# Kernel tuning notes

Measured on AMD Instinct MI355X. Metric: run time of the kernel, lower is better.

The kernel has to match this reference:

```python
import jax, jax.numpy as jnp
import numpy as np

N_NODES = 20000
N_EDGES = 100000
WALK_LEN = 4
FEAT_DIM = 256
HID = 64
NUM_HEAD = 8
H_RNN = NUM_HEAD * HID  # 512
OUT_DIM = 16


def setup_inputs() -> dict:
    key = jax.random.key(0)
    ks = jax.random.split(key, 12)
    s = 0.05  # small init scale for numerical stability
    return {
        "x": jax.random.normal(ks[0], (N_NODES, FEAT_DIM), jnp.float32),
        "W_mlp": jax.random.normal(ks[1], (HID, FEAT_DIM), jnp.float32) * s,
        "b_mlp": jnp.zeros((HID,), jnp.float32),
        "W_ih": jax.random.normal(ks[2], (3 * H_RNN, HID), jnp.float32) * s,
        "W_hh": jax.random.normal(ks[3], (3 * H_RNN, H_RNN), jnp.float32) * s,
        "b_ih": jnp.zeros((3 * H_RNN,), jnp.float32),
        "b_hh": jnp.zeros((3 * H_RNN,), jnp.float32),
        "attn": jax.random.normal(ks[4], (1, NUM_HEAD, HID), jnp.float32) * s,
        "W_emb": jax.random.normal(ks[5], (HID, H_RNN), jnp.float32) * s,
        "b_emb": jnp.zeros((HID,), jnp.float32),
        "W_last": jax.random.normal(ks[6], (OUT_DIM, HID), jnp.float32) * s,
        "b_last": jnp.zeros((OUT_DIM,), jnp.float32),
        "edge_metapath_indices": jax.random.randint(ks[7], (N_EDGES, WALK_LEN), 0, N_NODES),
        "num_nodes": N_NODES,
    }


def reference(x, W_mlp, b_mlp, W_ih, W_hh, b_ih, b_hh, attn, W_emb, b_emb,
              W_last, b_last, edge_metapath_indices, num_nodes):
    # self channel: embedding = mlp(data.x)
    emb = x @ W_mlp.T + b_mlp                       # [N, hid]

    # rnn channel: gather per-metapath node embeddings
    edata = emb[edge_metapath_indices]              # [E, L, hid]
    E = edata.shape[0]
    h_rnn = W_hh.shape[1]

    # torch nn.GRU cell (gate order r, z, n), scan over path length
    def gru_step(h, x_t):
        xg = x_t @ W_ih.T + b_ih                    # [E, 3H]
        hg = h @ W_hh.T + b_hh                      # [E, 3H]
        xr, xz, xn = jnp.split(xg, 3, axis=-1)
        hr, hz, hn = jnp.split(hg, 3, axis=-1)
        r = jax.nn.sigmoid(xr + hr)
        z = jax.nn.sigmoid(xz + hz)
        n = jnp.tanh(xn + r * hn)
        return (1.0 - z) * n + z * h, None

    h0 = jnp.zeros((E, h_rnn), edata.dtype)
    hT, _ = jax.lax.scan(gru_step, h0, jnp.swapaxes(edata, 0, 1))  # [E, 8*hid]

    num_head, hid = attn.shape[1], attn.shape[2]
    eft = hT.reshape(E, num_head, hid)              # per-edge features

    # attention logits + leaky_relu(0.01)
    a = jnp.sum(eft * attn, axis=-1)                # [E, num_head]
    a = jnp.where(a > 0, a, 0.01 * a)

    # edge softmax grouped by destination node (indices[:, -1])
    dst = edge_metapath_indices[:, -1]
    m = jax.ops.segment_max(a, dst, num_segments=num_nodes)        # [N, H]
    ea = jnp.exp(a - m[dst])
    ssum = jax.ops.segment_sum(ea, dst, num_segments=num_nodes)    # [N, H]
    alpha = ea / ssum[dst]                          # [E, H]

    # message passing: scatter-sum of attention-weighted edge features
    ft = jax.ops.segment_sum(eft * alpha[:, :, None], dst,
                             num_segments=num_nodes)               # [N, H, hid]
    ret = ft.reshape(num_nodes, num_head * hid)
    rnn_emb = ret @ W_emb.T + b_emb                 # [N, hid]

    out = rnn_emb @ W_last.T + b_last               # [N, out_dim]
    return out
```

## Files before the change

kernel.cpp:

```cpp
#include <hip/hip_runtime.h>
#include <hip/hip_bf16.h>
#include <cstdint>

#define N_NODES 20000
#define N_EDGES 100000
#define WALK 4
#define FDIM 256
#define HID 64
#define NHEAD 8
#define HR 512
#define OUTD 16

typedef __attribute__((ext_vector_type(8))) short bf16x8;
typedef __attribute__((ext_vector_type(8))) unsigned short u16x8;
typedef __attribute__((ext_vector_type(4))) float f32x4;

__device__ __forceinline__ float b2f(unsigned short u){
  union{float f; unsigned u;} x; x.u = ((unsigned)u)<<16; return x.f;
}
__device__ __forceinline__ unsigned short f2b(float f){
  union{float f; unsigned u;} x; x.f = f;
  unsigned r = x.u + 0x7FFFu + ((x.u>>16)&1u);
  return (unsigned short)(r>>16);
}
__device__ __forceinline__ float sigmoidf_(float v){ return 1.0f/(1.0f+__expf(-v)); }
__device__ __forceinline__ float tanh_c(float v){
  v = fminf(fmaxf(v, -15.f), 15.f);
  const float t2 = __expf(2.0f*v);
  return (t2 - 1.0f) / (t2 + 1.0f);
}

__device__ __forceinline__ void gload16(const void* g, void* l){
  __builtin_amdgcn_global_load_lds(
      (const __attribute__((address_space(1))) void*)(g),
      (__attribute__((address_space(3))) void*)(l),
      16, 0, 0);
}

__device__ __forceinline__ f32x4 mfma16(bf16x8 a, bf16x8 b, f32x4 c){
  return __builtin_amdgcn_mfma_f32_16x16x32_bf16(a, b, c, 0, 0, 0);
}

__launch_bounds__(256)
__global__ void emb_kernel(const float* __restrict__ x,
                           const float* __restrict__ Wm,
                           const float* __restrict__ bm,
                           unsigned short* __restrict__ emb_bf)
{
  __shared__ float xs[4][FDIM];
  const int tid = threadIdx.x;
  const int node0 = blockIdx.x * 4;
  {
    const int row = tid >> 6;
    const int k4  = (tid & 63) * 4;
    *reinterpret_cast<float4*>(&xs[row][k4]) =
      *reinterpret_cast<const float4*>(&x[(size_t)(node0+row)*FDIM + k4]);
  }
  __syncthreads();
  const int nn = tid >> 6, c = tid & 63;
  float acc = bm[c];
  const float* wr = &Wm[c*FDIM];
  #pragma unroll 8
  for (int k=0;k<FDIM;k+=4){
    const float4 w = *reinterpret_cast<const float4*>(&wr[k]);
    acc += xs[nn][k]*w.x + xs[nn][k+1]*w.y + xs[nn][k+2]*w.z + xs[nn][k+3]*w.w;
  }
  emb_bf[(size_t)(node0+nn)*HID + c] = f2b(acc);
}

__launch_bounds__(256)
__global__ void prep_kernel(const float* __restrict__ Whh,
                            const float* __restrict__ Wih,
                            const float* __restrict__ Wemb,
                            unsigned short* __restrict__ WhhP,
                            unsigned short* __restrict__ WihP,
                            unsigned short* __restrict__ WembP)
{
  const int t = blockIdx.x*256 + threadIdx.x;
  if (t < 8*192*512){
    const int k = t & 511;
    const int r = (t >> 9) % 192;
    const int db = t / 98304;
    const int f = r >> 4, fr = r & 15;
    const int g = f % 3, dgrp = f / 3;
    const int G = g*HR + db*64 + dgrp*16 + fr;
    const int kg = k >> 6, kw = k & 63;
    const int c = kw >> 3, o = kw & 7;
    const int ksrc = (kg<<6) + (((c ^ (r&7)) << 3) | o);
    WhhP[t] = f2b(Whh[(size_t)G*HR + ksrc]);
  }
  if (t < 8*192*64){
    const int k = t & 63;
    const int r = (t >> 6) % 192;
    const int db = t / 12288;
    const int f = r >> 4, fr = r & 15;
    const int g = f % 3, dgrp = f / 3;
    const int G = g*HR + db*64 + dgrp*16 + fr;
    const int c = k >> 3, o = k & 7;
    const int ksrc = (((c ^ (r&7)) << 3) | o);
    WihP[t] = f2b(Wih[(size_t)G*HID + ksrc]);
  }
  if (t < 64*512){
    const int k = t & 511;
    const int o = t >> 9;
    const int kg = k >> 6, kw = k & 63;
    const int c = kw >> 3, off = kw & 7;
    const int ksrc = (kg<<6) + (((c ^ (o&7)) << 3) | off);
    WembP[t] = f2b(Wemb[(size_t)o*HR + ksrc]);
  }
}

__launch_bounds__(512)
__global__ void xg_kernel(const unsigned short* __restrict__ emb_bf,
                          const unsigned short* __restrict__ WihP,
                          const float* __restrict__ b_ih,
                          const float* __restrict__ b_hh,
                          unsigned short* __restrict__ xnP,
                          unsigned short* __restrict__ h1n)
{
  __shared__ __align__(16) char smem[32768 + 24576];
  char* Ab = smem;
  char* Bb = smem + 32768;
  const int tid = threadIdx.x, lane = tid & 63, w = tid >> 6;
  const int wr = w >> 1, wn = w & 1;
  const int n0 = blockIdx.x * 256;
  const int db = blockIdx.y;

  #pragma unroll
  for (int j=0;j<4;++j){
    const int flat = j*512 + tid;
    const int row = flat >> 3, c = flat & 7;
    int n = n0 + row; if (n > N_NODES-1) n = N_NODES-1;
    gload16(emb_bf + ((size_t)n*HID + ((c ^ (row&7))<<3)), Ab + ((j*512 + w*64)<<4));
  }
  #pragma unroll
  for (int j=0;j<3;++j){
    const int flat = j*512 + tid;
    const int row = flat >> 3, c = flat & 7;
    gload16(WihP + ((size_t)(db*192 + row)*HID + c*8), Bb + ((j*512 + w*64)<<4));
  }
  asm volatile("s_waitcnt vmcnt(0)" ::: "memory");
  __builtin_amdgcn_s_barrier();

  f32x4 acc[4][6];
  #pragma unroll
  for (int m=0;m<4;++m)
    #pragma unroll
    for (int f=0;f<6;++f) acc[m][f] = (f32x4)(0.f);

  auto readFrag = [&](const char* base, int row, int kk)->bf16x8{
    const int chunk = (kk<<2) + (lane>>4);
    return *reinterpret_cast<const bf16x8*>(base + (row<<7) + ((chunk ^ (row&7))<<4));
  };
  #pragma unroll
  for (int kk=0; kk<2; ++kk){
    bf16x8 a_[4];
    #pragma unroll
    for (int mf=0; mf<4; ++mf) a_[mf] = readFrag(Ab, wr*64 + mf*16 + (lane&15), kk);
    #pragma unroll
    for (int nf=0; nf<6; ++nf){
      const bf16x8 b_ = readFrag(Bb, wn*96 + nf*16 + (lane&15), kk);
      #pragma unroll
      for (int mf=0; mf<4; ++mf) acc[mf][nf] = mfma16(a_[mf], b_, acc[mf][nf]);
    }
  }

  const int fr_ = lane & 15;
  #pragma unroll
  for (int mf=0; mf<4; ++mf){
    #pragma unroll
    for (int reg=0; reg<4; ++reg){
      const int row = wr*64 + mf*16 + ((lane>>4)<<2) + reg;
      const int n = n0 + row;
      if (n < N_NODES){
        #pragma unroll
        for (int t=0; t<2; ++t){
          const int d6 = (2*wn+t)*16 + fr_;
          const int dG = db*64 + d6;
          const float xr = acc[mf][t*3+0][reg] + b_ih[dG];
          const float xz = acc[mf][t*3+1][reg] + b_ih[HR+dG];
          const float xn = acc[mf][t*3+2][reg] + b_ih[2*HR+dG];
          xnP[((size_t)db*N_NODES + n)*64 + d6] = f2b(xn);
          const float r = sigmoidf_(xr + b_hh[dG]);
          const float z = sigmoidf_(xz + b_hh[HR+dG]);
          const float nn = tanh_c(xn + r*b_hh[2*HR+dG]);
          h1n[(size_t)n*HR + dG] = f2b((1.0f - z)*nn);
        }
      }
    }
  }
}

template<int STEP, bool SCORE>
__launch_bounds__(512, 2)
__global__ void gru_mfma(const unsigned short* __restrict__ emb_bf,
                         const int* __restrict__ idx,
                         const unsigned short* __restrict__ h_in,
                         unsigned short* __restrict__ h_out,
                         const unsigned short* __restrict__ WhhP,
                         const unsigned short* __restrict__ WihP,
                         const unsigned short* __restrict__ xnP,
                         const float* __restrict__ b_ih,
                         const float* __restrict__ b_hh,
                         const float* __restrict__ attn,
                         float* __restrict__ a_buf)
{
  constexpr bool GATHER = (STEP == 1);
  __shared__ __align__(16) char smem[3*32768 + 2*24576];

  const int tid = threadIdx.x;
  const int lane = tid & 63;
  const int w = tid >> 6;
  const int wr = w >> 1, wn = w & 1;

  const int bid = blockIdx.x;
  const int sid = (bid & 7)*391 + (bid >> 3);
  const int et = sid >> 3;
  const int db = sid & 7;
  const int e0 = et * 256;

  f32x4 acc[4][6];
  #pragma unroll
  for (int m=0;m<4;++m)
    #pragma unroll
    for (int f=0;f<6;++f) acc[m][f] = (f32x4)(0.f);

  auto Abase = [&](int s)->char*{ return smem + s*32768; };
  auto Bbase = [&](int s)->char*{ return smem + 98304 + s*24576; };

  auto stage_A = [&](int slot, int kt){
    #pragma unroll
    for (int j=0;j<4;++j){
      const int flat = j*512 + tid;
      const int row = flat >> 3, c = flat & 7;
      int e = e0 + row; if (e > N_EDGES-1) e = N_EDGES-1;
      const unsigned short* src;
      if (kt == 8){
        const int node = idx[e*WALK + STEP];
        src = emb_bf + ((size_t)node*HID + ((c ^ (row&7)) << 3));
      } else if (GATHER){
        const int node = idx[e*WALK];
        src = h_in + ((size_t)node*HR + kt*64 + ((c ^ (row&7)) << 3));
      } else {
        src = h_in + ((size_t)e*HR + kt*64 + c*8);
      }
      gload16(src, Abase(slot) + ((j*512 + w*64) << 4));
    }
  };
  auto stage_B = [&](int slot, int kt){
    #pragma unroll
    for (int j=0;j<3;++j){
      const int flat = j*512 + tid;
      const int row = flat >> 3, c = flat & 7;
      const unsigned short* src = (kt < 8)
        ? WhhP + ((size_t)(db*192 + row)*HR + kt*64 + c*8)
        : WihP + ((size_t)(db*192 + row)*HID + c*8);
      gload16(src, Bbase(slot) + ((j*512 + w*64) << 4));
    }
  };

  auto readFrag = [&](const char* base, int row, int kk)->bf16x8{
    const int chunk = (kk<<2) + (lane>>4);
    return *reinterpret_cast<const bf16x8*>(base + (row<<7) + ((chunk ^ (row&7))<<4));
  };

#define COMPUTE(ab, bb, kk, XS)                                               \
  {                                                                           \
    bf16x8 a_[4];                                                             \
    _Pragma("unroll")                                                         \
    for (int mf=0; mf<4; ++mf)                                                \
      a_[mf] = readFrag(ab, wr*64 + mf*16 + (lane&15), kk);                   \
    __builtin_amdgcn_s_setprio(1);                                            \
    _Pragma("unroll")                                                         \
    for (int nf=0; nf<6; ++nf){                                               \
      if (XS && (nf % 3) == 2) continue;                                      \
      const bf16x8 b_ = readFrag(bb, wn*96 + nf*16 + (lane&15), kk);          \
      _Pragma("unroll")                                                       \
      for (int mf=0; mf<4; ++mf)                                              \
        acc[mf][nf] = mfma16(a_[mf], b_, acc[mf][nf]);                        \
    }                                                                         \
    __builtin_amdgcn_s_setprio(0);                                            \
  }

  stage_A(0, 0); stage_B(0, 0); stage_A(1, 1);
  asm volatile("s_waitcnt vmcnt(4)" ::: "memory");
  __builtin_amdgcn_s_barrier();
  __builtin_amdgcn_sched_barrier(0);

  #pragma unroll
  for (int kt=0; kt<9; ++kt){
    char* ab = Abase(kt%3);
    char* bb = Bbase(kt&1);
    if (kt+1 < 9) stage_B((kt+1)&1, kt+1);
    if (kt==8){ COMPUTE(ab, bb, 0, true);  } else { COMPUTE(ab, bb, 0, false); }
    if (kt+2 < 9) stage_A((kt+2)%3, kt+2);
    if (kt==8){ COMPUTE(ab, bb, 1, true);  } else { COMPUTE(ab, bb, 1, false); }
    if (kt < 8){
      if (kt < 7) asm volatile("s_waitcnt vmcnt(4)" ::: "memory");
      else        asm volatile("s_waitcnt vmcnt(0)" ::: "memory");
      __builtin_amdgcn_s_barrier();
      __builtin_amdgcn_sched_barrier(0);
    }
  }
#undef COMPUTE

  const int fr_ = lane & 15;
  float bhr[2], bhz[2], bhn[2], at[2];
  #pragma unroll
  for (int t=0; t<2; ++t){
    const int d6 = (2*wn+t)*16 + fr_;
    const int dG = db*64 + d6;
    bhr[t] = b_ih[dG]      + b_hh[dG];
    bhz[t] = b_ih[HR+dG]   + b_hh[HR+dG];
    bhn[t] = b_hh[2*HR+dG];
    at[t]  = SCORE ? attn[db*HID + d6] : 0.f;
  }

  #pragma unroll
  for (int mf=0; mf<4; ++mf){
    #pragma unroll
    for (int reg=0; reg<4; ++reg){
      const int row = wr*64 + mf*16 + ((lane>>4)<<2) + reg;
      const int e = e0 + row;
      float sp = 0.f;
      if (e < N_EDGES){
        const int4 iv = *reinterpret_cast<const int4*>(&idx[e*WALK]);
        const int nodeS = (STEP==1) ? iv.y : ((STEP==2) ? iv.z : iv.w);
        #pragma unroll
        for (int t=0; t<2; ++t){
          const int d6 = (2*wn+t)*16 + fr_;
          const int dG = db*64 + d6;
          const float xn = b2f(xnP[((size_t)db*N_NODES + nodeS)*64 + d6]);
          float hold;
          if (GATHER) hold = b2f(h_in[(size_t)iv.x*HR + dG]);
          else        hold = b2f(h_in[(size_t)e*HR + db*64 + (((d6>>3) ^ (e&7))<<3) + (d6&7)]);
          const float r  = sigmoidf_(acc[mf][t*3+0][reg] + bhr[t]);
          const float z  = sigmoidf_(acc[mf][t*3+1][reg] + bhz[t]);
          const float hn = acc[mf][t*3+2][reg] + bhn[t];
          const float nn = tanh_c(xn + r*hn);
          const float hv = (1.0f - z)*nn + z*hold;
          h_out[(size_t)e*HR + db*64 + (((d6>>3) ^ (e&7))<<3) + (d6&7)] = f2b(hv);
          if (SCORE) sp += hv * at[t];
        }
      }
      if (SCORE){
        sp += __shfl_xor(sp, 1);
        sp += __shfl_xor(sp, 2);
        sp += __shfl_xor(sp, 4);
        sp += __shfl_xor(sp, 8);
        if (fr_ == 0 && e < N_EDGES)
          atomicAdd(&a_buf[e*NHEAD + db], sp);
      }
    }
  }
}

__launch_bounds__(256)
__global__ void score2_kernel(const int* __restrict__ idx,
                              float* __restrict__ a_buf,
                              unsigned int* __restrict__ mmax)
{
  const int flat = blockIdx.x*256 + threadIdx.x;
  const int e = flat >> 3, h = flat & 7;
  const float s = a_buf[flat];
  const float a = s > 0.f ? s : 0.01f*s;
  a_buf[flat] = a;
  const int dst = idx[e*WALK + 3];
  union{float f; unsigned u;} x; x.f = a;
  const unsigned key = (x.u & 0x80000000u) ? ~x.u : (x.u | 0x80000000u);
  atomicMax(&mmax[dst*NHEAD + h], key);
}

__launch_bounds__(256)
__global__ void ea_kernel(const int* __restrict__ idx,
                          float* __restrict__ a_buf,
                          const unsigned int* __restrict__ mmax,
                          float* __restrict__ ssum)
{
  const int flat = blockIdx.x*256 + threadIdx.x;
  const int e = flat >> 3, h = flat & 7;
  const int dst = idx[e*WALK + 3];
  const unsigned key = mmax[dst*NHEAD + h];
  union{float f; unsigned u;} x;
  x.u = (key & 0x80000000u) ? (key & 0x7FFFFFFFu) : ~key;
  const float ea = __expf(a_buf[flat] - x.f);
  a_buf[flat] = ea;
  atomicAdd(&ssum[dst*NHEAD + h], ea);
}

__launch_bounds__(256)
__global__ void alpha_kernel(const int* __restrict__ idx,
                             float* __restrict__ a_buf,
                             const float* __restrict__ ssum)
{
  const int flat = blockIdx.x*256 + threadIdx.x;
  const int e = flat >> 3, h = flat & 7;
  const int dst = idx[e*WALK + 3];
  a_buf[flat] = a_buf[flat] / ssum[dst*NHEAD + h];
}

__launch_bounds__(256)
__global__ void z_kernel(const unsigned short* __restrict__ hT,
                         const int* __restrict__ idx,
                         const float* __restrict__ alpha,
                         const unsigned short* __restrict__ WembP,
                         float* __restrict__ zacc)
{
  __shared__ __align__(16) char zs[40960];
  char* Az = zs;
  char* Bz = zs + 32768;
  const int tid = threadIdx.x;
  const int lane = tid & 63;
  const int w = tid >> 6;
  const int e0 = blockIdx.x * 256;

  f32x4 acc[4][4];
  #pragma unroll
  for (int m=0;m<4;++m)
    #pragma unroll
    for (int f=0;f<4;++f) acc[m][f] = (f32x4)(0.f);

  auto readFrag = [&](const char* base, int row, int kk)->bf16x8{
    const int chunk = (kk<<2) + (lane>>4);
    return *reinterpret_cast<const bf16x8*>(base + (row<<7) + ((chunk ^ (row&7))<<4));
  };

  #pragma unroll 1
  for (int kt=0; kt<8; ++kt){
    __syncthreads();
    #pragma unroll
    for (int j=0;j<8;++j){
      const int flat = j*256 + tid;
      const int row = flat >> 3, c = flat & 7;
      int e = e0 + row; if (e > N_EDGES-1) e = N_EDGES-1;
      const u16x8 hv = *reinterpret_cast<const u16x8*>(hT + (size_t)e*HR + kt*64 + c*8);
      const float al = alpha[e*NHEAD + kt];
      union { bf16x8 v; unsigned short s[8]; } o;
      #pragma unroll
      for (int i=0;i<8;++i) o.s[i] = f2b(b2f(hv[i]) * al);
      *reinterpret_cast<bf16x8*>(Az + flat*16) = o.v;
    }
    #pragma unroll
    for (int j=0;j<2;++j){
      const int flat = j*256 + tid;
      const int row = flat >> 3, c = flat & 7;
      gload16(WembP + ((size_t)row*HR + kt*64 + c*8), Bz + ((j*256 + w*64)<<4));
    }
    __syncthreads();
    #pragma unroll
    for (int kk=0; kk<2; ++kk){
      bf16x8 a_[4];
      #pragma unroll
      for (int mf=0; mf<4; ++mf)
        a_[mf] = readFrag(Az, w*64 + mf*16 + (lane&15), kk);
      #pragma unroll
      for (int nf=0; nf<4; ++nf){
        const bf16x8 b_ = readFrag(Bz, nf*16 + (lane&15), kk);
        #pragma unroll
        for (int mf=0; mf<4; ++mf)
          acc[mf][nf] = mfma16(a_[mf], b_, acc[mf][nf]);
      }
    }
  }

  #pragma unroll
  for (int mf=0; mf<4; ++mf){
    #pragma unroll
    for (int reg=0; reg<4; ++reg){
      const int row = w*64 + mf*16 + ((lane>>4)<<2) + reg;
      const int e = e0 + row;
      if (e < N_EDGES){
        const int dst = idx[e*WALK + 3];
        #pragma unroll
        for (int nf=0; nf<4; ++nf){
          const int o = nf*16 + (lane&15);
          atomicAdd(&zacc[(size_t)dst*64 + o], acc[mf][nf][reg]);
        }
      }
    }
  }
}

__launch_bounds__(256)
__global__ void out2_kernel(const float* __restrict__ zacc,
                            const float* __restrict__ b_emb,
                            const float* __restrict__ W_last,
                            const float* __restrict__ b_last,
                            float* __restrict__ out)
{
  const int flat = blockIdx.x*256 + threadIdx.x;
  if (flat >= N_NODES*OUTD) return;
  const int n = flat >> 4, o = flat & 15;
  float s = b_last[o];
  const float* zr = &zacc[(size_t)n*64];
  const float* wl = &W_last[o*64];
  #pragma unroll
  for (int k=0;k<64;++k) s += (zr[k] + b_emb[k]) * wl[k];
  out[(size_t)n*OUTD + o] = s;
}

extern "C" void kernel_launch(void* const* d_in, const int* in_sizes, int n_in,
                              void* d_out, int out_size, void* d_ws, size_t ws_size,
                              hipStream_t stream)
{
  (void)in_sizes; (void)n_in; (void)out_size; (void)ws_size;
  const float* x      = (const float*)d_in[0];
  const float* W_mlp  = (const float*)d_in[1];
  const float* b_mlp  = (const float*)d_in[2];
  const float* W_ih   = (const float*)d_in[3];
  const float* W_hh   = (const float*)d_in[4];
  const float* b_ih   = (const float*)d_in[5];
  const float* b_hh   = (const float*)d_in[6];
  const float* attn   = (const float*)d_in[7];
  const float* W_emb  = (const float*)d_in[8];
  const float* b_emb  = (const float*)d_in[9];
  const float* W_last = (const float*)d_in[10];
  const float* b_last = (const float*)d_in[11];
  const int*   idx    = (const int*)d_in[12];
  float* out = (float*)d_out;

  char* ws = (char*)d_ws;
  unsigned short* WhhP   = (unsigned short*)(ws + 0);
  unsigned short* WihP   = (unsigned short*)(ws + 1572864);
  unsigned short* WembP  = (unsigned short*)(ws + 1769472);
  unsigned short* emb_bf = (unsigned short*)(ws + 1835008);
  unsigned short* xnP    = (unsigned short*)(ws + 4395008);
  float*          a_buf  = (float*)(ws + 24875008);
  unsigned int*   mmax   = (unsigned int*)(ws + 28075008);
  float*          ssum   = (float*)(ws + 28715008);
  float*          zacc   = (float*)(ws + 29355008);
  unsigned short* h_a    = (unsigned short*)(ws + 34475008);
  unsigned short* h_b    = (unsigned short*)(ws + 136875008);
  unsigned short* h1n    = h_b;

  hipMemsetAsync(a_buf, 0, 9600000, stream);

  prep_kernel<<<3072, 256, 0, stream>>>(W_hh, W_ih, W_emb, WhhP, WihP, WembP);
  emb_kernel<<<N_NODES/4, 256, 0, stream>>>(x, W_mlp, b_mlp, emb_bf);

  dim3 xgrid(79, 8);
  xg_kernel<<<xgrid, 512, 0, stream>>>(emb_bf, WihP, b_ih, b_hh, xnP, h1n);

  const int NWG = 391*8;
  gru_mfma<1,false><<<NWG, 512, 0, stream>>>(emb_bf, idx, h1n, h_a, WhhP, WihP, xnP, b_ih, b_hh, attn, a_buf);
  gru_mfma<2,false><<<NWG, 512, 0, stream>>>(emb_bf, idx, h_a, h_b, WhhP, WihP, xnP, b_ih, b_hh, attn, a_buf);
  gru_mfma<3,true ><<<NWG, 512, 0, stream>>>(emb_bf, idx, h_b, h_a, WhhP, WihP, xnP, b_ih, b_hh, attn, a_buf);

  score2_kernel<<<N_EDGES*NHEAD/256, 256, 0, stream>>>(idx, a_buf, mmax);
  ea_kernel<<<N_EDGES*NHEAD/256, 256, 0, stream>>>(idx, a_buf, mmax, ssum);
  alpha_kernel<<<N_EDGES*NHEAD/256, 256, 0, stream>>>(idx, a_buf, ssum);
  z_kernel<<<391, 256, 0, stream>>>(h_a, idx, a_buf, WembP, zacc);
  out2_kernel<<<(N_NODES*OUTD+255)/256, 256, 0, stream>>>(zacc, b_emb, W_last, b_last, out);
}
```

Before: 1.299 ms.

## Retile GRU kernels to 128-edge single-buffer blocks and fuse alpha into z_kernel

Rewrites the GRU MFMA kernels from 256-edge, 512-thread blocks with a triple/double-buffered LDS pipeline to 128-edge, 256-thread blocks using one LDS buffer and __syncthreads between k-tiles. Gate weights are repacked so each wave holds contiguous r/z/n fragments, and gather indices are hoisted into registers. The score write becomes a plain store instead of an atomicAdd, and the separate alpha normalisation kernel is removed by dividing by ssum inside z_kernel. Dropping the software pipeline risks exposing global load latency, while smaller blocks may raise occupancy.

```diff
diff --git a/kernel.cpp b/kernel.cpp
--- a/kernel.cpp
+++ b/kernel.cpp
@@ -81,9 +81,7 @@
     const int k = t & 511;
     const int r = (t >> 9) % 192;
     const int db = t / 98304;
-    const int f = r >> 4, fr = r & 15;
-    const int g = f % 3, dgrp = f / 3;
-    const int G = g*HR + db*64 + dgrp*16 + fr;
+    const int G = (r>>6)*HR + db*64 + (r&63);
     const int kg = k >> 6, kw = k & 63;
     const int c = kw >> 3, o = kw & 7;
     const int ksrc = (kg<<6) + (((c ^ (r&7)) << 3) | o);
@@ -93,9 +91,7 @@
     const int k = t & 63;
     const int r = (t >> 6) % 192;
     const int db = t / 12288;
-    const int f = r >> 4, fr = r & 15;
-    const int g = f % 3, dgrp = f / 3;
-    const int G = g*HR + db*64 + dgrp*16 + fr;
+    const int G = (r>>6)*HR + db*64 + (r&63);
     const int c = k >> 3, o = k & 7;
     const int ksrc = (((c ^ (r&7)) << 3) | o);
     WihP[t] = f2b(Wih[(size_t)G*HID + ksrc]);
@@ -110,7 +106,7 @@
   }
 }
 
-__launch_bounds__(512)
+__launch_bounds__(256)
 __global__ void xg_kernel(const unsigned short* __restrict__ emb_bf,
                           const unsigned short* __restrict__ WihP,
                           const float* __restrict__ b_ih,
@@ -118,68 +114,65 @@
                           unsigned short* __restrict__ xnP,
                           unsigned short* __restrict__ h1n)
 {
-  __shared__ __align__(16) char smem[32768 + 24576];
-  char* Ab = smem;
-  char* Bb = smem + 32768;
+  __shared__ __align__(16) unsigned short As[128*64];
+  __shared__ __align__(16) unsigned short Bs[192*64];
   const int tid = threadIdx.x, lane = tid & 63, w = tid >> 6;
-  const int wr = w >> 1, wn = w & 1;
-  const int n0 = blockIdx.x * 256;
+  const int tx = lane & 15, ty = lane >> 4;
+  const int n0 = blockIdx.x * 128;
   const int db = blockIdx.y;
 
   #pragma unroll
   for (int j=0;j<4;++j){
-    const int flat = j*512 + tid;
+    const int flat = j*256 + tid;
     const int row = flat >> 3, c = flat & 7;
     int n = n0 + row; if (n > N_NODES-1) n = N_NODES-1;
-    gload16(emb_bf + ((size_t)n*HID + ((c ^ (row&7))<<3)), Ab + ((j*512 + w*64)<<4));
-  }
-  #pragma unroll
-  for (int j=0;j<3;++j){
-    const int flat = j*512 + tid;
+    gload16(emb_bf + ((size_t)n*HID + ((c ^ (row&7))<<3)), (char*)As + flat*16);
+  }
+  #pragma unroll
+  for (int j=0;j<6;++j){
+    const int flat = j*256 + tid;
     const int row = flat >> 3, c = flat & 7;
-    gload16(WihP + ((size_t)(db*192 + row)*HID + c*8), Bb + ((j*512 + w*64)<<4));
-  }
-  asm volatile("s_waitcnt vmcnt(0)" ::: "memory");
-  __builtin_amdgcn_s_barrier();
-
-  f32x4 acc[4][6];
-  #pragma unroll
-  for (int m=0;m<4;++m)
-    #pragma unroll
-    for (int f=0;f<6;++f) acc[m][f] = (f32x4)(0.f);
-
-  auto readFrag = [&](const char* base, int row, int kk)->bf16x8{
-    const int chunk = (kk<<2) + (lane>>4);
-    return *reinterpret_cast<const bf16x8*>(base + (row<<7) + ((chunk ^ (row&7))<<4));
+    gload16(WihP + ((size_t)(db*192 + row)*HID + c*8), (char*)Bs + flat*16);
+  }
+  __syncthreads();
+
+  f32x4 acc[2][12];
+  #pragma unroll
+  for (int m=0;m<2;++m)
+    #pragma unroll
+    for (int f=0;f<12;++f) acc[m][f] = (f32x4)(0.f);
+
+  auto readFrag = [&](const unsigned short* base, int row, int kk)->bf16x8{
+    const int chunk = (kk<<2) + ty;
+    return *reinterpret_cast<const bf16x8*>(
+        reinterpret_cast<const char*>(base) + (row<<7) + ((chunk ^ (row&7))<<4));
   };
   #pragma unroll
   for (int kk=0; kk<2; ++kk){
-    bf16x8 a_[4];
-    #pragma unroll
-    for (int mf=0; mf<4; ++mf) a_[mf] = readFrag(Ab, wr*64 + mf*16 + (lane&15), kk);
-    #pragma unroll
-    for (int nf=0; nf<6; ++nf){
-      const bf16x8 b_ = readFrag(Bb, wn*96 + nf*16 + (lane&15), kk);
-      #pragma unroll
-      for (int mf=0; mf<4; ++mf) acc[mf][nf] = mfma16(a_[mf], b_, acc[mf][nf]);
-    }
-  }
-
-  const int fr_ = lane & 15;
-  #pragma unroll
-  for (int mf=0; mf<4; ++mf){
+    const bf16x8 a0 = readFrag(As, w*32 + tx, kk);
+    const bf16x8 a1 = readFrag(As, w*32 + 16 + tx, kk);
+    #pragma unroll
+    for (int nf=0; nf<12; ++nf){
+      const bf16x8 b = readFrag(Bs, nf*16 + tx, kk);
+      acc[0][nf] = mfma16(a0, b, acc[0][nf]);
+      acc[1][nf] = mfma16(a1, b, acc[1][nf]);
+    }
+  }
+
+  #pragma unroll
+  for (int m=0;m<2;++m){
     #pragma unroll
     for (int reg=0; reg<4; ++reg){
-      const int row = wr*64 + mf*16 + ((lane>>4)<<2) + reg;
+      const int row = w*32 + m*16 + ty*4 + reg;
       const int n = n0 + row;
       if (n < N_NODES){
         #pragma unroll
-        for (int t=0; t<2; ++t){
-          const int d6 = (2*wn+t)*16 + fr_;
+        for (int fr=0; fr<4; ++fr){
+          const int d6 = fr*16 + tx;
           const int dG = db*64 + d6;
-          const float xr = acc[mf][t*3+0][reg] + b_ih[dG];
-          const float xz = acc[mf][t*3+1][reg] + b_ih[HR+dG];
-          const float xn = acc[mf][t*3+2][reg] + b_ih[2*HR+dG];
+          const float xr = acc[m][fr][reg]   + b_ih[dG];
+          const float xz = acc[m][4+fr][reg] + b_ih[HR+dG];
+          const float xn = acc[m][8+fr][reg] + b_ih[2*HR+dG];
           xnP[((size_t)db*N_NODES + n)*64 + d6] = f2b(xn);
           const float r = sigmoidf_(xr + b_hh[dG]);
           const float z = sigmoidf_(xz + b_hh[HR+dG]);
@@ -192,7 +185,7 @@
 }
 
 template<int STEP, bool SCORE>
-__launch_bounds__(512, 2)
+__launch_bounds__(256)
 __global__ void gru_mfma(const unsigned short* __restrict__ emb_bf,
                          const int* __restrict__ idx,
                          const unsigned short* __restrict__ h_in,
@@ -206,141 +199,124 @@
                          float* __restrict__ a_buf)
 {
   constexpr bool GATHER = (STEP == 1);
-  __shared__ __align__(16) char smem[3*32768 + 2*24576];
-
-  const int tid = threadIdx.x;
-  const int lane = tid & 63;
-  const int w = tid >> 6;
-  const int wr = w >> 1, wn = w & 1;
+  __shared__ __align__(16) unsigned short As[128*64];
+  __shared__ __align__(16) unsigned short Bs[192*64];
+
+  const int tid = threadIdx.x, lane = tid & 63, w = tid >> 6;
+  const int tx = lane & 15, ty = lane >> 4;
 
   const int bid = blockIdx.x;
-  const int sid = (bid & 7)*391 + (bid >> 3);
+  const int sid = (bid & 7)*782 + (bid >> 3);
   const int et = sid >> 3;
   const int db = sid & 7;
-  const int e0 = et * 256;
-
-  f32x4 acc[4][6];
-  #pragma unroll
-  for (int m=0;m<4;++m)
-    #pragma unroll
-    for (int f=0;f<6;++f) acc[m][f] = (f32x4)(0.f);
-
-  auto Abase = [&](int s)->char*{ return smem + s*32768; };
-  auto Bbase = [&](int s)->char*{ return smem + 98304 + s*24576; };
-
-  auto stage_A = [&](int slot, int kt){
+  const int e0 = et * 128;
+
+  int eS[4], nH[4], nX[4];
+  #pragma unroll
+  for (int j=0;j<4;++j){
+    int e = e0 + ((j*256 + tid) >> 3);
+    if (e > N_EDGES-1) e = N_EDGES-1;
+    eS[j] = e;
+    nX[j] = idx[e*WALK + STEP];
+    nH[j] = GATHER ? idx[e*WALK] : 0;
+  }
+
+  f32x4 acc[2][12];
+  #pragma unroll
+  for (int m=0;m<2;++m)
+    #pragma unroll
+    for (int f=0;f<12;++f) acc[m][f] = (f32x4)(0.f);
+
+  auto stageA = [&](int kt){
     #pragma unroll
     for (int j=0;j<4;++j){
-      const int flat = j*512 + tid;
+      const int flat = j*256 + tid;
       const int row = flat >> 3, c = flat & 7;
-      int e = e0 + row; if (e > N_EDGES-1) e = N_EDGES-1;
       const unsigned short* src;
       if (kt == 8){
-        const int node = idx[e*WALK + STEP];
-        src = emb_bf + ((size_t)node*HID + ((c ^ (row&7)) << 3));
+        src = emb_bf + ((size_t)nX[j]*HID + ((c ^ (row&7)) << 3));
       } else if (GATHER){
-        const int node = idx[e*WALK];
-        src = h_in + ((size_t)node*HR + kt*64 + ((c ^ (row&7)) << 3));
+        src = h_in + ((size_t)nH[j]*HR + kt*64 + ((c ^ (row&7)) << 3));
       } else {
-        src = h_in + ((size_t)e*HR + kt*64 + c*8);
-      }
-      gload16(src, Abase(slot) + ((j*512 + w*64) << 4));
+        src = h_in + ((size_t)eS[j]*HR + kt*64 + c*8);
+      }
+      gload16(src, (char*)As + flat*16);
     }
   };
-  auto stage_B = [&](int slot, int kt){
-    #pragma unroll
-    for (int j=0;j<3;++j){
-      const int flat = j*512 + tid;
+  auto stageB = [&](int kt){
+    #pragma unroll
+    for (int j=0;j<6;++j){
+      const int flat = j*256 + tid;
       const int row = flat >> 3, c = flat & 7;
       const unsigned short* src = (kt < 8)
         ? WhhP + ((size_t)(db*192 + row)*HR + kt*64 + c*8)
         : WihP + ((size_t)(db*192 + row)*HID + c*8);
-      gload16(src, Bbase(slot) + ((j*512 + w*64) << 4));
+      gload16(src, (char*)Bs + flat*16);
     }
   };
-
-  auto readFrag = [&](const char* base, int row, int kk)->bf16x8{
-    const int chunk = (kk<<2) + (lane>>4);
-    return *reinterpret_cast<const bf16x8*>(base + (row<<7) + ((chunk ^ (row&7))<<4));
+  auto readFrag = [&](const unsigned short* base, int row, int kk)->bf16x8{
+    const int chunk = (kk<<2) + ty;
+    return *reinterpret_cast<const bf16x8*>(
+        reinterpret_cast<const char*>(base) + (row<<7) + ((chunk ^ (row&7))<<4));
   };
 
-#define COMPUTE(ab, bb, kk, XS)                                               \
-  {                                                                           \
-    bf16x8 a_[4];                                                             \
-    _Pragma("unroll")                                                         \
-    for (int mf=0; mf<4; ++mf)                                                \
-      a_[mf] = readFrag(ab, wr*64 + mf*16 + (lane&15), kk);                   \
-    __builtin_amdgcn_s_setprio(1);                                            \
-    _Pragma("unroll")                                                         \
-    for (int nf=0; nf<6; ++nf){                                               \
-      if (XS && (nf % 3) == 2) continue;                                      \
-      const bf16x8 b_ = readFrag(bb, wn*96 + nf*16 + (lane&15), kk);          \
-      _Pragma("unroll")                                                       \
-      for (int mf=0; mf<4; ++mf)                                              \
-        acc[mf][nf] = mfma16(a_[mf], b_, acc[mf][nf]);                        \
-    }                                                                         \
-    __builtin_amdgcn_s_setprio(0);                                            \
-  }
-
-  stage_A(0, 0); stage_B(0, 0); stage_A(1, 1);
-  asm volatile("s_waitcnt vmcnt(4)" ::: "memory");
-  __builtin_amdgcn_s_barrier();
-  __builtin_amdgcn_sched_barrier(0);
+  stageA(0); stageB(0);
 
   #pragma unroll
   for (int kt=0; kt<9; ++kt){
-    char* ab = Abase(kt%3);
-    char* bb = Bbase(kt&1);
-    if (kt+1 < 9) stage_B((kt+1)&1, kt+1);
-    if (kt==8){ COMPUTE(ab, bb, 0, true);  } else { COMPUTE(ab, bb, 0, false); }
-    if (kt+2 < 9) stage_A((kt+2)%3, kt+2);
-    if (kt==8){ COMPUTE(ab, bb, 1, true);  } else { COMPUTE(ab, bb, 1, false); }
+    __syncthreads();
+    #pragma unroll
+    for (int kk=0; kk<2; ++kk){
+      const bf16x8 a0 = readFrag(As, w*32 + tx, kk);
+      const bf16x8 a1 = readFrag(As, w*32 + 16 + tx, kk);
+      #pragma unroll
+      for (int nf=0; nf<12; ++nf){
+        if (kt == 8 && nf >= 8) continue;
+        const bf16x8 b = readFrag(Bs, nf*16 + tx, kk);
+        acc[0][nf] = mfma16(a0, b, acc[0][nf]);
+        acc[1][nf] = mfma16(a1, b, acc[1][nf]);
+      }
+    }
     if (kt < 8){
-      if (kt < 7) asm volatile("s_waitcnt vmcnt(4)" ::: "memory");
-      else        asm volatile("s_waitcnt vmcnt(0)" ::: "memory");
-      __builtin_amdgcn_s_barrier();
-      __builtin_amdgcn_sched_barrier(0);
-    }
-  }
-#undef COMPUTE
-
-  const int fr_ = lane & 15;
-  float bhr[2], bhz[2], bhn[2], at[2];
-  #pragma unroll
-  for (int t=0; t<2; ++t){
-    const int d6 = (2*wn+t)*16 + fr_;
-    const int dG = db*64 + d6;
-    bhr[t] = b_ih[dG]      + b_hh[dG];
-    bhz[t] = b_ih[HR+dG]   + b_hh[HR+dG];
-    bhn[t] = b_hh[2*HR+dG];
-    at[t]  = SCORE ? attn[db*HID + d6] : 0.f;
-  }
-
-  #pragma unroll
-  for (int mf=0; mf<4; ++mf){
+      __syncthreads();
+      stageA(kt+1); stageB(kt+1);
+    }
+  }
+
+  float bir[4], biz[4], bhn[4], atv[4];
+  #pragma unroll
+  for (int fr=0; fr<4; ++fr){
+    const int dG = db*64 + fr*16 + tx;
+    bir[fr] = b_ih[dG]      + b_hh[dG];
+    biz[fr] = b_ih[HR+dG]   + b_hh[HR+dG];
+    bhn[fr] = b_hh[2*HR+dG];
+    atv[fr] = SCORE ? attn[dG] : 0.f;
+  }
+
+  #pragma unroll
+  for (int m=0;m<2;++m){
     #pragma unroll
     for (int reg=0; reg<4; ++reg){
-      const int row = wr*64 + mf*16 + ((lane>>4)<<2) + reg;
+      const int row = w*32 + m*16 + ty*4 + reg;
       const int e = e0 + row;
       float sp = 0.f;
       if (e < N_EDGES){
-        const int4 iv = *reinterpret_cast<const int4*>(&idx[e*WALK]);
-        const int nodeS = (STEP==1) ? iv.y : ((STEP==2) ? iv.z : iv.w);
+        const int nodeS = idx[e*WALK + STEP];
+        const int nodeH = GATHER ? idx[e*WALK] : 0;
         #pragma unroll
-        for (int t=0; t<2; ++t){
-          const int d6 = (2*wn+t)*16 + fr_;
+        for (int fr=0; fr<4; ++fr){
+          const int d6 = fr*16 + tx;
           const int dG = db*64 + d6;
           const float xn = b2f(xnP[((size_t)db*N_NODES + nodeS)*64 + d6]);
           float hold;
-          if (GATHER) hold = b2f(h_in[(size_t)iv.x*HR + dG]);
+          if (GATHER) hold = b2f(h_in[(size_t)nodeH*HR + dG]);
           else        hold = b2f(h_in[(size_t)e*HR + db*64 + (((d6>>3) ^ (e&7))<<3) + (d6&7)]);
-          const float r  = sigmoidf_(acc[mf][t*3+0][reg] + bhr[t]);
-          const float z  = sigmoidf_(acc[mf][t*3+1][reg] + bhz[t]);
-          const float hn = acc[mf][t*3+2][reg] + bhn[t];
-          const float nn = tanh_c(xn + r*hn);
+          const float r  = sigmoidf_(acc[m][fr][reg]   + bir[fr]);
+          const float z  = sigmoidf_(acc[m][4+fr][reg] + biz[fr]);
+          const float nn = tanh_c(xn + r*(acc[m][8+fr][reg] + bhn[fr]));
           const float hv = (1.0f - z)*nn + z*hold;
           h_out[(size_t)e*HR + db*64 + (((d6>>3) ^ (e&7))<<3) + (d6&7)] = f2b(hv);
-          if (SCORE) sp += hv * at[t];
+          if (SCORE) sp += hv * atv[fr];
         }
       }
       if (SCORE){
@@ -348,8 +324,7 @@
         sp += __shfl_xor(sp, 2);
         sp += __shfl_xor(sp, 4);
         sp += __shfl_xor(sp, 8);
-        if (fr_ == 0 && e < N_EDGES)
-          atomicAdd(&a_buf[e*NHEAD + db], sp);
+        if (tx == 0 && e < N_EDGES) a_buf[e*NHEAD + db] = sp;
       }
     }
   }
@@ -389,20 +364,10 @@
 }
 
 __launch_bounds__(256)
-__global__ void alpha_kernel(const int* __restrict__ idx,
-                             float* __restrict__ a_buf,
-                             const float* __restrict__ ssum)
-{
-  const int flat = blockIdx.x*256 + threadIdx.x;
-  const int e = flat >> 3, h = flat & 7;
-  const int dst = idx[e*WALK + 3];
-  a_buf[flat] = a_buf[flat] / ssum[dst*NHEAD + h];
-}
-
-__launch_bounds__(256)
 __global__ void z_kernel(const unsigned short* __restrict__ hT,
                          const int* __restrict__ idx,
-                         const float* __restrict__ alpha,
+                         const float* __restrict__ ea_buf,
+                         const float* __restrict__ ssum,
                          const unsigned short* __restrict__ WembP,
                          float* __restrict__ zacc)
 {
@@ -414,6 +379,15 @@
   const int w = tid >> 6;
   const int e0 = blockIdx.x * 256;
 
+  int ej[8], dstj[8];
+  #pragma unroll
+  for (int j=0;j<8;++j){
+    int e = e0 + ((j*256 + tid) >> 3);
+    if (e > N_EDGES-1) e = N_EDGES-1;
+    ej[j] = e;
+    dstj[j] = idx[e*WALK + 3];
+  }
+
   f32x4 acc[4][4];
   #pragma unroll
   for (int m=0;m<4;++m)
@@ -431,10 +405,9 @@
     #pragma unroll
     for (int j=0;j<8;++j){
       const int flat = j*256 + tid;
-      const int row = flat >> 3, c = flat & 7;
-      int e = e0 + row; if (e > N_EDGES-1) e = N_EDGES-1;
-      const u16x8 hv = *reinterpret_cast<const u16x8*>(hT + (size_t)e*HR + kt*64 + c*8);
-      const float al = alpha[e*NHEAD + kt];
+      const int e = ej[j];
+      const u16x8 hv = *reinterpret_cast<const u16x8*>(hT + (size_t)e*HR + kt*64 + (flat&7)*8);
+      const float al = ea_buf[e*NHEAD + kt] / ssum[dstj[j]*NHEAD + kt];
       union { bf16x8 v; unsigned short s[8]; } o;
       #pragma unroll
       for (int i=0;i<8;++i) o.s[i] = f2b(b2f(hv[i]) * al);
@@ -538,17 +511,16 @@
   prep_kernel<<<3072, 256, 0, stream>>>(W_hh, W_ih, W_emb, WhhP, WihP, WembP);
   emb_kernel<<<N_NODES/4, 256, 0, stream>>>(x, W_mlp, b_mlp, emb_bf);
 
-  dim3 xgrid(79, 8);
-  xg_kernel<<<xgrid, 512, 0, stream>>>(emb_bf, WihP, b_ih, b_hh, xnP, h1n);
-
-  const int NWG = 391*8;
-  gru_mfma<1,false><<<NWG, 512, 0, stream>>>(emb_bf, idx, h1n, h_a, WhhP, WihP, xnP, b_ih, b_hh, attn, a_buf);
-  gru_mfma<2,false><<<NWG, 512, 0, stream>>>(emb_bf, idx, h_a, h_b, WhhP, WihP, xnP, b_ih, b_hh, attn, a_buf);
-  gru_mfma<3,true ><<<NWG, 512, 0, stream>>>(emb_bf, idx, h_b, h_a, WhhP, WihP, xnP, b_ih, b_hh, attn, a_buf);
+  dim3 xgrid((N_NODES + 127)/128, 8);
+  xg_kernel<<<xgrid, 256, 0, stream>>>(emb_bf, WihP, b_ih, b_hh, xnP, h1n);
+
+  const int NWG = 782*8;
+  gru_mfma<1,false><<<NWG, 256, 0, stream>>>(emb_bf, idx, h1n, h_a, WhhP, WihP, xnP, b_ih, b_hh, attn, a_buf);
+  gru_mfma<2,false><<<NWG, 256, 0, stream>>>(emb_bf, idx, h_a, h_b, WhhP, WihP, xnP, b_ih, b_hh, attn, a_buf);
+  gru_mfma<3,true ><<<NWG, 256, 0, stream>>>(emb_bf, idx, h_b, h_a, WhhP, WihP, xnP, b_ih, b_hh, attn, a_buf);
 
   score2_kernel<<<N_EDGES*NHEAD/256, 256, 0, stream>>>(idx, a_buf, mmax);
   ea_kernel<<<N_EDGES*NHEAD/256, 256, 0, stream>>>(idx, a_buf, mmax, ssum);
-  alpha_kernel<<<N_EDGES*NHEAD/256, 256, 0, stream>>>(idx, a_buf, ssum);
-  z_kernel<<<391, 256, 0, stream>>>(h_a, idx, a_buf, WembP, zacc);
+  z_kernel<<<391, 256, 0, stream>>>(h_a, idx, a_buf, ssum, WembP, zacc);
   out2_kernel<<<(N_NODES*OUTD+255)/256, 256, 0, stream>>>(zacc, b_emb, W_last, b_last, out);
 }
```

New measurement: 1.184 ms. 1.1x faster.
